# Performance work log

Hardware: AMD Instinct MI355X
Metric: run time of the kernel (lower is better)

## Reference

```python
import jax, jax.numpy as jnp
import numpy as np

B, T, D = 4, 1024, 256
H, DK, C = 8, 32, 16  # n_heads, d_key, pos-encoder hidden units
DV = D // H
NEG = -1e15
EPS_SM = 1e-5
EPS_LN = 1e-5
SLOPE = 0.01  # LeakyReLU default


def setup_inputs() -> dict:
    key = jax.random.key(0)
    ks = jax.random.split(key, 16)
    s = 0.05
    x = jax.random.normal(ks[0], (B, T, D), jnp.float32)
    src_mask = jax.random.randint(ks[1], (B, T, T), 0, 2).astype(bool)
    rel_dists = jax.random.uniform(ks[2], (B, 1, T, T), jnp.float32)
    Wq = jax.random.normal(ks[3], (H, DK, D), jnp.float32) * s
    Wk = jax.random.normal(ks[4], (H, DK, D), jnp.float32) * s
    Wv = jax.random.normal(ks[5], (H, DV, D), jnp.float32) * s
    pw1 = jax.random.normal(ks[6], (H, C), jnp.float32) * s
    pb1 = jax.random.normal(ks[7], (H, C), jnp.float32) * s
    pw2 = jax.random.normal(ks[8], (H, C), jnp.float32) * s
    pb2 = jax.random.normal(ks[9], (H,), jnp.float32) * s
    Wo = jax.random.normal(ks[10], (D, D), jnp.float32) * s
    bo = jax.random.normal(ks[11], (D,), jnp.float32) * s
    Wf = jax.random.normal(ks[12], (D, D), jnp.float32) * s
    bf = jax.random.normal(ks[13], (D,), jnp.float32) * s
    g1 = jnp.ones((D,), jnp.float32)
    beta1 = jnp.zeros((D,), jnp.float32)
    g2 = jnp.ones((D,), jnp.float32)
    beta2 = jnp.zeros((D,), jnp.float32)
    return dict(x=x, src_mask=src_mask, rel_dists=rel_dists, Wq=Wq, Wk=Wk, Wv=Wv,
                pw1=pw1, pb1=pb1, pw2=pw2, pb2=pb2, Wo=Wo, bo=bo, Wf=Wf, bf=bf,
                g1=g1, beta1=beta1, g2=g2, beta2=beta2)


def _l2norm(v):
    # F.normalize(p=2, dim=-1): v / max(||v||, 1e-12)
    n = jnp.sqrt(jnp.sum(v * v, axis=-1, keepdims=True))
    return v / jnp.maximum(n, 1e-12)


def _lrelu(h):
    return jnp.where(h >= 0, h, SLOPE * h)


def _pos_bias(d, pw1, pb1, pw2, pb2):
    # d: [B,T,T]; per-head 1x1-conv MLP applied elementwise.
    # Loop over the tiny channel dim (16) to avoid a [B,H,T,T,C] intermediate.
    bias = jnp.broadcast_to(pb2[None, :, None, None], (d.shape[0], pw1.shape[0], d.shape[1], d.shape[2]))
    for c in range(pw1.shape[1]):
        h = d[:, None] * pw1[None, :, c, None, None] + pb1[None, :, c, None, None]
        bias = bias + pw2[None, :, c, None, None] * _lrelu(h)
    return bias  # [B,H,T,T]


def _layer_norm(v, g, b):
    mu = jnp.mean(v, axis=-1, keepdims=True)
    var = jnp.mean((v - mu) ** 2, axis=-1, keepdims=True)
    return (v - mu) * jax.lax.rsqrt(var + EPS_LN) * g + b


def reference(x, src_mask, rel_dists, Wq, Wk, Wv, pw1, pb1, pw2, pb2,
              Wo, bo, Wf, bf, g1, beta1, g2, beta2):
    # cosine-normalized multi-head attention (all heads batched)
    q = _l2norm(jnp.einsum('btd,hkd->bhtk', x, Wq))
    k = _l2norm(jnp.einsum('bsd,hkd->bhsk', x, Wk))
    v = jnp.einsum('bsd,hvd->bhsv', x, Wv)
    logits = jnp.einsum('bhtk,bhsk->bhts', q, k)
    logits = logits - _pos_bias(rel_dists[:, 0], pw1, pb1, pw2, pb2)
    logits = jnp.where(src_mask[:, None], NEG, logits)
    # custom softmax: exp / (sum + 1e-5) (handles all-padded rows)
    z = jnp.exp(logits)
    attn = z / (jnp.sum(z, axis=-1, keepdims=True) + EPS_SM)
    heads = jnp.einsum('bhts,bhsv->bhtv', attn, v)
    y = heads.transpose(0, 2, 1, 3).reshape(x.shape[0], x.shape[1], -1)  # concat heads
    y = y @ Wo.T + bo
    # residual + LN + FFN (dropout is identity in eval mode)
    zz = _layer_norm(x + y, g1, beta1)
    z_ff = _lrelu(zz @ Wf.T + bf)
    return _layer_norm(zz + z_ff, g2, beta2)
```

## Files before the change

kernel.cpp:

```cpp
#include <hip/hip_runtime.h>
#include <math.h>

#define Tc 1024
#define Dc 256
#define Hc 8
#define Cc 16
#define LUTN 256

typedef __attribute__((ext_vector_type(8))) short short8;
typedef __attribute__((ext_vector_type(4))) float f32x4;

__device__ __forceinline__ unsigned bf16u(float x) {
    unsigned u = __float_as_uint(x);
    return (u + 0x7FFFu + ((u >> 16) & 1u)) >> 16;
}
__device__ __forceinline__ unsigned pk2(float lo, float hi) {
    return bf16u(lo) | (bf16u(hi) << 16);
}
__device__ __forceinline__ unsigned pk2t(float lo, float hi) {
    return __builtin_amdgcn_perm(__float_as_uint(hi), __float_as_uint(lo), 0x07060302u);
}
__device__ __forceinline__ float upk(unsigned v) { return __uint_as_float(v << 16); }
__device__ __forceinline__ float upkh(unsigned v) { return __uint_as_float(v & 0xffff0000u); }

__device__ __forceinline__ short8 packW8(const float* __restrict__ p) {
    float4 b0 = *(const float4*)(p);
    float4 b1 = *(const float4*)(p + 4);
    union { short8 s; unsigned wds[4]; } B;
    B.wds[0] = pk2(b0.x, b0.y); B.wds[1] = pk2(b0.z, b0.w);
    B.wds[2] = pk2(b1.x, b1.y); B.wds[3] = pk2(b1.z, b1.w);
    return B.s;
}

__global__ __launch_bounds__(256) void pack_dm(
    const float* __restrict__ rel, const int* __restrict__ msk,
    ushort* __restrict__ Dm)
{
    const int idx = (blockIdx.x * 256 + threadIdx.x) * 8;
    float4 d0 = *(const float4*)(rel + idx);
    float4 d1 = *(const float4*)(rel + idx + 4);
    int4   m0 = *(const int4*)(msk + idx);
    int4   m1 = *(const int4*)(msk + idx + 4);
    uint4 p;
    p.x = (m0.x ? 0xBF80u : bf16u(d0.x)) | ((m0.y ? 0xBF80u : bf16u(d0.y)) << 16);
    p.y = (m0.z ? 0xBF80u : bf16u(d0.z)) | ((m0.w ? 0xBF80u : bf16u(d0.w)) << 16);
    p.z = (m1.x ? 0xBF80u : bf16u(d1.x)) | ((m1.y ? 0xBF80u : bf16u(d1.y)) << 16);
    p.w = (m1.z ? 0xBF80u : bf16u(d1.z)) | ((m1.w ? 0xBF80u : bf16u(d1.w)) << 16);
    *(uint4*)(Dm + idx) = p;
}

__global__ __launch_bounds__(256) void qkv_direct(
    const float* __restrict__ x,
    const float* __restrict__ Wq, const float* __restrict__ Wk,
    const float* __restrict__ Wv,
    ushort* __restrict__ Qb, ushort* __restrict__ Kb, ushort* __restrict__ Vt)
{
    const int tid = threadIdx.x;
    const int w = tid >> 6;
    const int l = tid & 63;
    const int u = l & 15, g = l >> 4;
    const int rbase = blockIdx.x * 16;
    const int cb = (blockIdx.y * 4 + w) * 64;
    const int mat = cb >> 8;
    const int fcb = cb & 255;
    const float* Wmat = (mat == 0) ? Wq : (mat == 1) ? Wk : Wv;

    f32x4 acc[4];
#pragma unroll
    for (int nt = 0; nt < 4; ++nt) acc[nt] = (f32x4){0.f, 0.f, 0.f, 0.f};

    const float* arow = x + (size_t)(rbase + u) * 256 + g * 8;
#pragma unroll 2
    for (int k0 = 0; k0 < 256; k0 += 32) {
        short8 af = packW8(arow + k0);
#pragma unroll
        for (int nt = 0; nt < 4; ++nt) {
            short8 bfr = packW8(Wmat + (size_t)(fcb + nt * 16 + u) * 256 + k0 + g * 8);
            acc[nt] = __builtin_amdgcn_mfma_f32_16x16x32_bf16(af, bfr, acc[nt], 0, 0, 0);
        }
    }

    if (mat < 2) {
        ushort* Out = (mat == 0) ? Qb : Kb;
#pragma unroll
        for (int hp = 0; hp < 2; ++hp) {
            const int head = (fcb >> 5) + hp;
#pragma unroll
            for (int reg = 0; reg < 4; ++reg) {
                float ss = acc[2 * hp][reg] * acc[2 * hp][reg]
                         + acc[2 * hp + 1][reg] * acc[2 * hp + 1][reg];
                ss += __shfl_xor(ss, 1, 64);
                ss += __shfl_xor(ss, 2, 64);
                ss += __shfl_xor(ss, 4, 64);
                ss += __shfl_xor(ss, 8, 64);
                float scn = 1.f / fmaxf(sqrtf(ss), 1e-12f);
                const int t = rbase + 4 * g + reg;
                const int bb = t >> 10, tt = t & 1023;
                const size_t base = ((size_t)(bb * 8 + head) * Tc + tt) * 32;
                Out[base + u]      = (ushort)bf16u(acc[2 * hp][reg] * scn);
                Out[base + 16 + u] = (ushort)bf16u(acc[2 * hp + 1][reg] * scn);
            }
        }
    } else {
#pragma unroll
        for (int nt = 0; nt < 4; ++nt) {
            const int head = (fcb >> 5) + (nt >> 1);
            const int vt = nt & 1;
#pragma unroll
            for (int reg = 0; reg < 4; ++reg) {
                const int s = rbase + 4 * g + reg;
                const int bb = s >> 10, ss = s & 1023;
                const int bh = bb * 8 + head;
                Vt[(((size_t)bh * 32 + (ss >> 5)) * 2 + vt) * 512 + u * 32 + (ss & 31)] =
                    (ushort)bf16u(acc[nt][reg]);
            }
        }
    }
}

__global__ __launch_bounds__(256) void attn_mfma(
    const ushort* __restrict__ Qb, const ushort* __restrict__ Kb,
    const ushort* __restrict__ Vt, const ushort* __restrict__ Dm,
    const float* __restrict__ pw1, const float* __restrict__ pb1,
    const float* __restrict__ pw2, const float* __restrict__ pb2,
    ushort* __restrict__ Yb)
{
    const int tid = threadIdx.x;
    const int w = tid >> 6;
    const int l = tid & 63;
    const int u = l & 15;
    const int g = l >> 4;
    const int bid = blockIdx.x;
    const int c   = bid & 7;
    const int hg  = (bid >> 3) & 3;
    const int tb  = (bid >> 5) * 8 + c;
    const int t0  = (tb & 63) * 16;
    const int b   = tb >> 6;

    __shared__ __align__(16) ushort lut_s[1024];
    __shared__ __align__(16) ushort comb[4 * 16 * 72];
    __shared__ float rs_s[8 * 16];

    {
        const int bin = tid;
        const float d0 = bin * (1.f / LUTN), d1 = (bin + 1) * (1.f / LUTN);
#pragma unroll
        for (int hp = 0; hp < 2; ++hp) {
            const int h = hg * 2 + hp;
            float y0 = pb2[h], y1 = pb2[h];
#pragma unroll
            for (int cc = 0; cc < Cc; ++cc) {
                float w1 = pw1[h * Cc + cc], b1 = pb1[h * Cc + cc], w2 = pw2[h * Cc + cc];
                float h0 = fmaf(w1, d0, b1), h1 = fmaf(w1, d1, b1);
                y0 = fmaf(w2, h0 >= 0.f ? h0 : 0.01f * h0, y0);
                y1 = fmaf(w2, h1 >= 0.f ? h1 : 0.01f * h1, y1);
            }
            float a = (y1 - y0) * (float)LUTN;
            float bq = y0 - a * d0;
            lut_s[bin * 4 + hp * 2]     = (ushort)bf16u(a);
            lut_s[bin * 4 + hp * 2 + 1] = (ushort)bf16u(bq);
        }
    }

    const int bh0 = b * 8 + hg * 2;
    short8 qf[2];
#pragma unroll
    for (int hi = 0; hi < 2; ++hi)
        qf[hi] = *(const short8*)(Qb + (((size_t)(bh0 + hi) * Tc + t0 + u) * 32 + g * 8));

    const short8 ones = (short8){0x3F80, 0x3F80, 0x3F80, 0x3F80,
                                 0x3F80, 0x3F80, 0x3F80, 0x3F80};

    f32x4 oacc[2][2];
    f32x4 rsacc[2];
#pragma unroll
    for (int hi = 0; hi < 2; ++hi) {
        oacc[hi][0] = (f32x4){0.f, 0.f, 0.f, 0.f};
        oacc[hi][1] = (f32x4){0.f, 0.f, 0.f, 0.f};
        rsacc[hi]   = (f32x4){0.f, 0.f, 0.f, 0.f};
    }

    __syncthreads();

    const int s_begin = w * 256;
    const ushort* drow = Dm + (size_t)b * Tc * Tc + (size_t)(t0 + u) * Tc;

    uint4 dmv = *(const uint4*)(drow + s_begin + 8 * g);
    short8 kc[2][2];
#pragma unroll
    for (int hi = 0; hi < 2; ++hi) {
        const size_t kb = ((size_t)(bh0 + hi) * Tc + s_begin + 2 * u) * 32 + g * 8;
        kc[hi][0] = *(const short8*)(Kb + kb);
        kc[hi][1] = *(const short8*)(Kb + kb + 32);
    }

    for (int sc = s_begin; sc < s_begin + 256; sc += 32) {
        const int nx = (sc + 32 < s_begin + 256) ? sc + 32 : s_begin;
        uint4 dmn = *(const uint4*)(drow + nx + 8 * g);
        short8 kn[2][2];
#pragma unroll
        for (int hi = 0; hi < 2; ++hi) {
            const size_t kb = ((size_t)(bh0 + hi) * Tc + nx + 2 * u) * 32 + g * 8;
            kn[hi][0] = *(const short8*)(Kb + kb);
            kn[hi][1] = *(const short8*)(Kb + kb + 32);
        }

        const unsigned dw[4] = {dmv.x, dmv.y, dmv.z, dmv.w};
        float dA[4], dB[4];
#pragma unroll
        for (int j = 0; j < 4; ++j) {
            dA[j] = upk(dw[j]);
            dB[j] = upkh(dw[j]);
        }
        float biasA[4][2], biasB[4][2];
#pragma unroll
        for (int j = 0; j < 4; ++j) {
            int iA = (int)(dA[j] * (float)LUTN);
            int iB = (int)(dB[j] * (float)LUTN);
            iA = iA < 0 ? 0 : (iA > LUTN - 1 ? LUTN - 1 : iA);
            iB = iB < 0 ? 0 : (iB > LUTN - 1 ? LUTN - 1 : iB);
            uint2 wA = *(const uint2*)(lut_s + iA * 4);
            uint2 wB = *(const uint2*)(lut_s + iB * 4);
            biasA[j][0] = fmaf(upk(wA.x), dA[j], upkh(wA.x));
            biasA[j][1] = fmaf(upk(wA.y), dA[j], upkh(wA.y));
            biasB[j][0] = fmaf(upk(wB.x), dB[j], upkh(wB.x));
            biasB[j][1] = fmaf(upk(wB.y), dB[j], upkh(wB.y));
        }
#pragma unroll
        for (int hi = 0; hi < 2; ++hi) {
            const f32x4 z4 = (f32x4){0.f, 0.f, 0.f, 0.f};
            f32x4 sA = __builtin_amdgcn_mfma_f32_16x16x32_bf16(kc[hi][0], qf[hi], z4, 0, 0, 0);
            f32x4 sB = __builtin_amdgcn_mfma_f32_16x16x32_bf16(kc[hi][1], qf[hi], z4, 0, 0, 0);
            union { short8 s; unsigned w4[4]; } P;
#pragma unroll
            for (int j = 0; j < 4; ++j) {
                float zA = (dA[j] < 0.f) ? 0.f : __expf(sA[j] - biasA[j][hi]);
                float zB = (dB[j] < 0.f) ? 0.f : __expf(sB[j] - biasB[j][hi]);
                P.w4[j] = pk2t(zA, zB);
            }
            const ushort* vb = Vt + ((size_t)(bh0 + hi) * 32 + (sc >> 5)) * 1024;
            short8 vf0 = *(const short8*)(vb + u * 32 + g * 8);
            short8 vf1 = *(const short8*)(vb + 512 + u * 32 + g * 8);
            oacc[hi][0] = __builtin_amdgcn_mfma_f32_16x16x32_bf16(P.s, vf0, oacc[hi][0], 0, 0, 0);
            oacc[hi][1] = __builtin_amdgcn_mfma_f32_16x16x32_bf16(P.s, vf1, oacc[hi][1], 0, 0, 0);
            rsacc[hi]   = __builtin_amdgcn_mfma_f32_16x16x32_bf16(P.s, ones, rsacc[hi], 0, 0, 0);
        }
        dmv = dmn;
#pragma unroll
        for (int hi = 0; hi < 2; ++hi) {
            kc[hi][0] = kn[hi][0];
            kc[hi][1] = kn[hi][1];
        }
    }

#pragma unroll
    for (int hi = 0; hi < 2; ++hi)
        if (u == 0) {
#pragma unroll
            for (int reg = 0; reg < 4; ++reg)
                rs_s[(w * 2 + hi) * 16 + 4 * g + reg] = rsacc[hi][reg];
        }
#pragma unroll
    for (int hi = 0; hi < 2; ++hi)
#pragma unroll
        for (int vt = 0; vt < 2; ++vt)
#pragma unroll
            for (int reg = 0; reg < 4; ++reg)
                comb[w * 1152 + (4 * g + reg) * 72 + hi * 32 + vt * 16 + u] =
                    (ushort)(__float_as_uint(oacc[hi][vt][reg]) >> 16);
    __syncthreads();

    if (tid < 128) {
        const int tl = tid >> 3;
        const int f0 = (tid & 7) * 8;
        const int hl = f0 >> 5;
        float rstot = rs_s[hl * 16 + tl] + rs_s[(2 + hl) * 16 + tl]
                    + rs_s[(4 + hl) * 16 + tl] + rs_s[(6 + hl) * 16 + tl];
        float inv = 1.f / (rstot + 1e-5f);
        float o[8];
#pragma unroll
        for (int k = 0; k < 8; ++k) o[k] = 0.f;
#pragma unroll
        for (int ww = 0; ww < 4; ++ww) {
            uint4 pv = *(const uint4*)&comb[ww * 1152 + tl * 72 + f0];
            o[0] += upk(pv.x); o[1] += upkh(pv.x);
            o[2] += upk(pv.y); o[3] += upkh(pv.y);
            o[4] += upk(pv.z); o[5] += upkh(pv.z);
            o[6] += upk(pv.w); o[7] += upkh(pv.w);
        }
        uint4 pwv;
        pwv.x = pk2(o[0] * inv, o[1] * inv); pwv.y = pk2(o[2] * inv, o[3] * inv);
        pwv.z = pk2(o[4] * inv, o[5] * inv); pwv.w = pk2(o[6] * inv, o[7] * inv);
        *(uint4*)(Yb + ((size_t)b * Tc + t0 + tl) * Dc + hg * 64 + f0) = pwv;
    }
}

__global__ __launch_bounds__(512) void out_fused(
    const ushort* __restrict__ Yb, const float* __restrict__ Wo,
    const float* __restrict__ bo, const float* __restrict__ x,
    const float* __restrict__ g1, const float* __restrict__ be1,
    const float* __restrict__ Wf, const float* __restrict__ bfb,
    const float* __restrict__ g2, const float* __restrict__ be2,
    float* __restrict__ out)
{
    const int tid = threadIdx.x;
    const int w = tid >> 6;
    const int l = tid & 63;
    const int u = l & 15, g = l >> 4;
    const int rbase = blockIdx.x * 16;

    __shared__ float red1[128], red2[128];
    __shared__ __align__(16) ushort ZZs[16 * 256];

    f32x4 acc[2];
    acc[0] = (f32x4){0.f, 0.f, 0.f, 0.f};
    acc[1] = (f32x4){0.f, 0.f, 0.f, 0.f};
    const ushort* arow = Yb + (size_t)(rbase + u) * 256 + g * 8;
#pragma unroll 2
    for (int k0 = 0; k0 < 256; k0 += 32) {
        short8 af = *(const short8*)(arow + k0);
#pragma unroll
        for (int nt = 0; nt < 2; ++nt) {
            short8 bfr = packW8(Wo + (size_t)(w * 32 + nt * 16 + u) * 256 + k0 + g * 8);
            acc[nt] = __builtin_amdgcn_mfma_f32_16x16x32_bf16(af, bfr, acc[nt], 0, 0, 0);
        }
    }

    float bv[2];
#pragma unroll
    for (int nt = 0; nt < 2; ++nt) bv[nt] = bo[w * 32 + nt * 16 + u];

    float sv[4][2];
#pragma unroll
    for (int reg = 0; reg < 4; ++reg) {
        const int row = rbase + 4 * g + reg;
        float s1 = 0.f, s2 = 0.f;
#pragma unroll
        for (int nt = 0; nt < 2; ++nt) {
            const int col = w * 32 + nt * 16 + u;
            float s = acc[nt][reg] + bv[nt] + x[(size_t)row * 256 + col];
            sv[reg][nt] = s;
            s1 += s;
            s2 = fmaf(s, s, s2);
        }
        s1 += __shfl_xor(s1, 1, 64); s2 += __shfl_xor(s2, 1, 64);
        s1 += __shfl_xor(s1, 2, 64); s2 += __shfl_xor(s2, 2, 64);
        s1 += __shfl_xor(s1, 4, 64); s2 += __shfl_xor(s2, 4, 64);
        s1 += __shfl_xor(s1, 8, 64); s2 += __shfl_xor(s2, 8, 64);
        if (u == 0) { red1[w * 16 + 4 * g + reg] = s1; red2[w * 16 + 4 * g + reg] = s2; }
    }
    __syncthreads();

    float zzv[4][2];
#pragma unroll
    for (int reg = 0; reg < 4; ++reg) {
        const int rl = 4 * g + reg;
        float S1 = 0.f, S2 = 0.f;
#pragma unroll
        for (int ww = 0; ww < 8; ++ww) { S1 += red1[ww * 16 + rl]; S2 += red2[ww * 16 + rl]; }
        float mu = S1 * (1.f / 256.f);
        float var = S2 * (1.f / 256.f) - mu * mu;
        float rsig = rsqrtf(var + 1e-5f);
#pragma unroll
        for (int nt = 0; nt < 2; ++nt) {
            const int col = w * 32 + nt * 16 + u;
            float zz = (sv[reg][nt] - mu) * rsig * g1[col] + be1[col];
            zzv[reg][nt] = zz;
            const int boff = (rl * 512 + col * 2) ^ ((rl & 7) << 4);
            *(ushort*)((char*)ZZs + boff) = (ushort)bf16u(zz);
        }
    }
    __syncthreads();

    f32x4 acc2[2];
    acc2[0] = (f32x4){0.f, 0.f, 0.f, 0.f};
    acc2[1] = (f32x4){0.f, 0.f, 0.f, 0.f};
#pragma unroll 2
    for (int k0 = 0; k0 < 256; k0 += 32) {
        const int aoff = (u * 512 + (k0 + g * 8) * 2) ^ ((u & 7) << 4);
        short8 af = *(const short8*)((const char*)ZZs + aoff);
#pragma unroll
        for (int nt = 0; nt < 2; ++nt) {
            short8 bfr = packW8(Wf + (size_t)(w * 32 + nt * 16 + u) * 256 + k0 + g * 8);
            acc2[nt] = __builtin_amdgcn_mfma_f32_16x16x32_bf16(af, bfr, acc2[nt], 0, 0, 0);
        }
    }

    float bv2[2];
#pragma unroll
    for (int nt = 0; nt < 2; ++nt) bv2[nt] = bfb[w * 32 + nt * 16 + u];

    float sv2[4][2];
#pragma unroll
    for (int reg = 0; reg < 4; ++reg) {
        float s1 = 0.f, s2 = 0.f;
#pragma unroll
        for (int nt = 0; nt < 2; ++nt) {
            float v = acc2[nt][reg] + bv2[nt];
            v = v >= 0.f ? v : 0.01f * v;
            float s = v + zzv[reg][nt];
            sv2[reg][nt] = s;
            s1 += s;
            s2 = fmaf(s, s, s2);
        }
        s1 += __shfl_xor(s1, 1, 64); s2 += __shfl_xor(s2, 1, 64);
        s1 += __shfl_xor(s1, 2, 64); s2 += __shfl_xor(s2, 2, 64);
        s1 += __shfl_xor(s1, 4, 64); s2 += __shfl_xor(s2, 4, 64);
        s1 += __shfl_xor(s1, 8, 64); s2 += __shfl_xor(s2, 8, 64);
        if (u == 0) { red1[w * 16 + 4 * g + reg] = s1; red2[w * 16 + 4 * g + reg] = s2; }
    }
    __syncthreads();

#pragma unroll
    for (int reg = 0; reg < 4; ++reg) {
        const int row = rbase + 4 * g + reg;
        const int rl = 4 * g + reg;
        float S1 = 0.f, S2 = 0.f;
#pragma unroll
        for (int ww = 0; ww < 8; ++ww) { S1 += red1[ww * 16 + rl]; S2 += red2[ww * 16 + rl]; }
        float mu = S1 * (1.f / 256.f);
        float var = S2 * (1.f / 256.f) - mu * mu;
        float rsig = rsqrtf(var + 1e-5f);
#pragma unroll
        for (int nt = 0; nt < 2; ++nt) {
            const int col = w * 32 + nt * 16 + u;
            out[(size_t)row * 256 + col] = (sv2[reg][nt] - mu) * rsig * g2[col] + be2[col];
        }
    }
}

extern "C" void kernel_launch(void* const* d_in, const int* in_sizes, int n_in,
                              void* d_out, int out_size, void* d_ws, size_t ws_size,
                              hipStream_t stream) {
    const float* x    = (const float*)d_in[0];
    const int*   mask = (const int*)d_in[1];
    const float* rel  = (const float*)d_in[2];
    const float* Wq   = (const float*)d_in[3];
    const float* Wk   = (const float*)d_in[4];
    const float* Wv   = (const float*)d_in[5];
    const float* pw1  = (const float*)d_in[6];
    const float* pb1  = (const float*)d_in[7];
    const float* pw2  = (const float*)d_in[8];
    const float* pb2  = (const float*)d_in[9];
    const float* Wo   = (const float*)d_in[10];
    const float* bo   = (const float*)d_in[11];
    const float* Wf   = (const float*)d_in[12];
    const float* bf   = (const float*)d_in[13];
    const float* g1   = (const float*)d_in[14];
    const float* be1  = (const float*)d_in[15];
    const float* g2   = (const float*)d_in[16];
    const float* be2  = (const float*)d_in[17];
    float* out = (float*)d_out;

    char* wsb = (char*)d_ws;
    ushort* Qb = (ushort*)(wsb);
    ushort* Kb = (ushort*)(wsb + (size_t)(2 << 20));
    ushort* Vt = (ushort*)(wsb + (size_t)(4 << 20));
    ushort* Yb = (ushort*)(wsb + (size_t)(6 << 20));
    ushort* Dm = (ushort*)(wsb + (size_t)(8 << 20));

    pack_dm<<<2048, 256, 0, stream>>>(rel, mask, Dm);
    qkv_direct<<<dim3(256, 3), 256, 0, stream>>>(x, Wq, Wk, Wv, Qb, Kb, Vt);
    attn_mfma<<<1024, 256, 0, stream>>>(Qb, Kb, Vt, Dm,
                                        pw1, pb1, pw2, pb2, Yb);
    out_fused<<<256, 512, 0, stream>>>(Yb, Wo, bo, x, g1, be1,
                                       Wf, bf, g2, be2, out);
}
```

Measured before the change: 192.9 us.

## Fuse rel/mask packing into attention kernel with all heads per block

Removes the separate pack_dm kernel and its intermediate bf16 distance/mask buffer. Each 1024-thread attention block now covers all 8 heads for a 16-row query tile, loads the fp32 rel_dists and int mask rows once, and packs them into a swizzled shared-memory tile that every head reuses. This is meant to cut the global write and reread of the packed buffer and one launch. In exchange it uses far more LDS per block, reduces the grid to 256 blocks, and drops the register prefetch of the distance data.

```diff
diff --git a/kernel.cpp b/kernel.cpp
--- a/kernel.cpp
+++ b/kernel.cpp
@@ -30,23 +30,6 @@
     B.wds[0] = pk2(b0.x, b0.y); B.wds[1] = pk2(b0.z, b0.w);
     B.wds[2] = pk2(b1.x, b1.y); B.wds[3] = pk2(b1.z, b1.w);
     return B.s;
-}
-
-__global__ __launch_bounds__(256) void pack_dm(
-    const float* __restrict__ rel, const int* __restrict__ msk,
-    ushort* __restrict__ Dm)
-{
-    const int idx = (blockIdx.x * 256 + threadIdx.x) * 8;
-    float4 d0 = *(const float4*)(rel + idx);
-    float4 d1 = *(const float4*)(rel + idx + 4);
-    int4   m0 = *(const int4*)(msk + idx);
-    int4   m1 = *(const int4*)(msk + idx + 4);
-    uint4 p;
-    p.x = (m0.x ? 0xBF80u : bf16u(d0.x)) | ((m0.y ? 0xBF80u : bf16u(d0.y)) << 16);
-    p.y = (m0.z ? 0xBF80u : bf16u(d0.z)) | ((m0.w ? 0xBF80u : bf16u(d0.w)) << 16);
-    p.z = (m1.x ? 0xBF80u : bf16u(d1.x)) | ((m1.y ? 0xBF80u : bf16u(d1.y)) << 16);
-    p.w = (m1.z ? 0xBF80u : bf16u(d1.z)) | ((m1.w ? 0xBF80u : bf16u(d1.w)) << 16);
-    *(uint4*)(Dm + idx) = p;
 }
 
 __global__ __launch_bounds__(256) void qkv_direct(
@@ -118,9 +101,10 @@
     }
 }
 
-__global__ __launch_bounds__(256) void attn_mfma(
+__global__ __launch_bounds__(1024) void attn_fused(
     const ushort* __restrict__ Qb, const ushort* __restrict__ Kb,
-    const ushort* __restrict__ Vt, const ushort* __restrict__ Dm,
+    const ushort* __restrict__ Vt,
+    const float* __restrict__ rel, const int* __restrict__ msk,
     const float* __restrict__ pw1, const float* __restrict__ pb1,
     const float* __restrict__ pw2, const float* __restrict__ pb2,
     ushort* __restrict__ Yb)
@@ -132,21 +116,22 @@
     const int g = l >> 4;
     const int bid = blockIdx.x;
     const int c   = bid & 7;
-    const int hg  = (bid >> 3) & 3;
-    const int tb  = (bid >> 5) * 8 + c;
-    const int t0  = (tb & 63) * 16;
-    const int b   = tb >> 6;
-
-    __shared__ __align__(16) ushort lut_s[1024];
-    __shared__ __align__(16) ushort comb[4 * 16 * 72];
-    __shared__ float rs_s[8 * 16];
+    const int b   = c >> 1;
+    const int tt  = (bid >> 3) * 2 + (c & 1);
+    const int t0  = tt * 16;
+
+    __shared__ __align__(16) ushort dm_s[16 * 1024];
+    __shared__ __align__(16) ushort lut_s[256 * 16];
+    __shared__ __align__(16) ushort comb[16 * 16 * 64];
+    __shared__ float rs_s[16 * 2 * 16];
 
     {
-        const int bin = tid;
-        const float d0 = bin * (1.f / LUTN), d1 = (bin + 1) * (1.f / LUTN);
+        const int bin = tid & 255;
+        const int hb  = (tid >> 8) * 2;
 #pragma unroll
         for (int hp = 0; hp < 2; ++hp) {
-            const int h = hg * 2 + hp;
+            const int h = hb + hp;
+            const float d0 = bin * (1.f / LUTN), d1 = (bin + 1) * (1.f / LUTN);
             float y0 = pb2[h], y1 = pb2[h];
 #pragma unroll
             for (int cc = 0; cc < Cc; ++cc) {
@@ -157,12 +142,35 @@
             }
             float a = (y1 - y0) * (float)LUTN;
             float bq = y0 - a * d0;
-            lut_s[bin * 4 + hp * 2]     = (ushort)bf16u(a);
-            lut_s[bin * 4 + hp * 2 + 1] = (ushort)bf16u(bq);
-        }
-    }
-
-    const int bh0 = b * 8 + hg * 2;
+            lut_s[bin * 16 + h * 2]     = (ushort)bf16u(a);
+            lut_s[bin * 16 + h * 2 + 1] = (ushort)bf16u(bq);
+        }
+    }
+
+    {
+        const int row = tid >> 6;
+        const int lc  = tid & 63;
+        const float* rrow = rel + ((size_t)b * Tc + t0 + row) * Tc;
+        const int*   mrow = msk + ((size_t)b * Tc + t0 + row) * Tc;
+        const int swz = (row & 7) << 4;
+#pragma unroll
+        for (int i = 0; i < 2; ++i) {
+            const int s0 = lc * 8 + i * 512;
+            float4 d0v = *(const float4*)(rrow + s0);
+            float4 d1v = *(const float4*)(rrow + s0 + 4);
+            int4   m0v = *(const int4*)(mrow + s0);
+            int4   m1v = *(const int4*)(mrow + s0 + 4);
+            uint4 p;
+            p.x = (m0v.x ? 0xBF80u : bf16u(d0v.x)) | ((m0v.y ? 0xBF80u : bf16u(d0v.y)) << 16);
+            p.y = (m0v.z ? 0xBF80u : bf16u(d0v.z)) | ((m0v.w ? 0xBF80u : bf16u(d0v.w)) << 16);
+            p.z = (m1v.x ? 0xBF80u : bf16u(d1v.x)) | ((m1v.y ? 0xBF80u : bf16u(d1v.y)) << 16);
+            p.w = (m1v.z ? 0xBF80u : bf16u(d1v.z)) | ((m1v.w ? 0xBF80u : bf16u(d1v.w)) << 16);
+            *(uint4*)((char*)dm_s + ((row * 2048 + s0 * 2) ^ swz)) = p;
+        }
+    }
+
+    const int hgp = w >> 2;
+    const int bh0 = b * 8 + hgp * 2;
     short8 qf[2];
 #pragma unroll
     for (int hi = 0; hi < 2; ++hi)
@@ -182,10 +190,9 @@
 
     __syncthreads();
 
-    const int s_begin = w * 256;
-    const ushort* drow = Dm + (size_t)b * Tc * Tc + (size_t)(t0 + u) * Tc;
-
-    uint4 dmv = *(const uint4*)(drow + s_begin + 8 * g);
+    const int s_begin = (w & 3) * 256;
+    const int dswz = (u & 7) << 4;
+
     short8 kc[2][2];
 #pragma unroll
     for (int hi = 0; hi < 2; ++hi) {
@@ -196,7 +203,6 @@
 
     for (int sc = s_begin; sc < s_begin + 256; sc += 32) {
         const int nx = (sc + 32 < s_begin + 256) ? sc + 32 : s_begin;
-        uint4 dmn = *(const uint4*)(drow + nx + 8 * g);
         short8 kn[2][2];
 #pragma unroll
         for (int hi = 0; hi < 2; ++hi) {
@@ -205,6 +211,7 @@
             kn[hi][1] = *(const short8*)(Kb + kb + 32);
         }
 
+        uint4 dmv = *(const uint4*)((const char*)dm_s + ((u * 2048 + (sc + 8 * g) * 2) ^ dswz));
         const unsigned dw[4] = {dmv.x, dmv.y, dmv.z, dmv.w};
         float dA[4], dB[4];
 #pragma unroll
@@ -219,8 +226,8 @@
             int iB = (int)(dB[j] * (float)LUTN);
             iA = iA < 0 ? 0 : (iA > LUTN - 1 ? LUTN - 1 : iA);
             iB = iB < 0 ? 0 : (iB > LUTN - 1 ? LUTN - 1 : iB);
-            uint2 wA = *(const uint2*)(lut_s + iA * 4);
-            uint2 wB = *(const uint2*)(lut_s + iB * 4);
+            uint2 wA = *(const uint2*)(lut_s + iA * 16 + hgp * 4);
+            uint2 wB = *(const uint2*)(lut_s + iB * 16 + hgp * 4);
             biasA[j][0] = fmaf(upk(wA.x), dA[j], upkh(wA.x));
             biasA[j][1] = fmaf(upk(wA.y), dA[j], upkh(wA.y));
             biasB[j][0] = fmaf(upk(wB.x), dB[j], upkh(wB.x));
@@ -245,7 +252,6 @@
             oacc[hi][1] = __builtin_amdgcn_mfma_f32_16x16x32_bf16(P.s, vf1, oacc[hi][1], 0, 0, 0);
             rsacc[hi]   = __builtin_amdgcn_mfma_f32_16x16x32_bf16(P.s, ones, rsacc[hi], 0, 0, 0);
         }
-        dmv = dmn;
 #pragma unroll
         for (int hi = 0; hi < 2; ++hi) {
             kc[hi][0] = kn[hi][0];
@@ -266,23 +272,27 @@
         for (int vt = 0; vt < 2; ++vt)
 #pragma unroll
             for (int reg = 0; reg < 4; ++reg)
-                comb[w * 1152 + (4 * g + reg) * 72 + hi * 32 + vt * 16 + u] =
+                comb[w * 1024 + (4 * g + reg) * 64 + hi * 32 + vt * 16 + u] =
                     (ushort)(__float_as_uint(oacc[hi][vt][reg]) >> 16);
     __syncthreads();
 
-    if (tid < 128) {
-        const int tl = tid >> 3;
-        const int f0 = (tid & 7) * 8;
-        const int hl = f0 >> 5;
-        float rstot = rs_s[hl * 16 + tl] + rs_s[(2 + hl) * 16 + tl]
-                    + rs_s[(4 + hl) * 16 + tl] + rs_s[(6 + hl) * 16 + tl];
+    if (tid < 512) {
+        const int tl = tid >> 5;
+        const int f0 = (tid & 31) * 8;
+        const int hgp2 = f0 >> 6;
+        const int hi = (f0 >> 5) & 1;
+        const int w0 = hgp2 * 4;
+        float rstot = rs_s[((w0 + 0) * 2 + hi) * 16 + tl]
+                    + rs_s[((w0 + 1) * 2 + hi) * 16 + tl]
+                    + rs_s[((w0 + 2) * 2 + hi) * 16 + tl]
+                    + rs_s[((w0 + 3) * 2 + hi) * 16 + tl];
         float inv = 1.f / (rstot + 1e-5f);
         float o[8];
 #pragma unroll
         for (int k = 0; k < 8; ++k) o[k] = 0.f;
 #pragma unroll
-        for (int ww = 0; ww < 4; ++ww) {
-            uint4 pv = *(const uint4*)&comb[ww * 1152 + tl * 72 + f0];
+        for (int q = 0; q < 4; ++q) {
+            uint4 pv = *(const uint4*)&comb[(w0 + q) * 1024 + tl * 64 + (f0 & 63)];
             o[0] += upk(pv.x); o[1] += upkh(pv.x);
             o[2] += upk(pv.y); o[3] += upkh(pv.y);
             o[4] += upk(pv.z); o[5] += upkh(pv.z);
@@ -291,7 +301,7 @@
         uint4 pwv;
         pwv.x = pk2(o[0] * inv, o[1] * inv); pwv.y = pk2(o[2] * inv, o[3] * inv);
         pwv.z = pk2(o[4] * inv, o[5] * inv); pwv.w = pk2(o[6] * inv, o[7] * inv);
-        *(uint4*)(Yb + ((size_t)b * Tc + t0 + tl) * Dc + hg * 64 + f0) = pwv;
+        *(uint4*)(Yb + ((size_t)b * Tc + t0 + tl) * Dc + f0) = pwv;
     }
 }
 
@@ -457,12 +467,10 @@
     ushort* Kb = (ushort*)(wsb + (size_t)(2 << 20));
     ushort* Vt = (ushort*)(wsb + (size_t)(4 << 20));
     ushort* Yb = (ushort*)(wsb + (size_t)(6 << 20));
-    ushort* Dm = (ushort*)(wsb + (size_t)(8 << 20));
-
-    pack_dm<<<2048, 256, 0, stream>>>(rel, mask, Dm);
+
     qkv_direct<<<dim3(256, 3), 256, 0, stream>>>(x, Wq, Wk, Wv, Qb, Kb, Vt);
-    attn_mfma<<<1024, 256, 0, stream>>>(Qb, Kb, Vt, Dm,
-                                        pw1, pb1, pw2, pb2, Yb);
+    attn_fused<<<256, 1024, 0, stream>>>(Qb, Kb, Vt, rel, mask,
+                                         pw1, pb1, pw2, pb2, Yb);
     out_fused<<<256, 512, 0, stream>>>(Yb, Wo, bo, x, g1, be1,
                                        Wf, bf, g2, be2, out);
 }
```

Result: faster. 186.7 us (-3.2%).
